# Optimization experiments

Hardware: AMD Instinct MI355X
Metric: run time of the kernel (lower is better)

## Reference

```python
import jax, jax.numpy as jnp
import numpy as np

B, S, D, H = 2, 2048, 1024, 16
DK = D // H


def setup_inputs() -> dict:
    key = jax.random.key(0)
    ks = jax.random.split(key, 11)
    std = 1.0 / np.sqrt(D)
    inp = {
        "query": jax.random.normal(ks[0], (B, S, D), jnp.float32),
        "key": jax.random.normal(ks[1], (B, S, D), jnp.float32),
        "value": jax.random.normal(ks[2], (B, S, D), jnp.float32),
        # True = masked position (torch masked_fill semantics); causal mask
        "mask": jnp.triu(jnp.ones((1, 1, S, S), jnp.bool_), k=1),
        "Wq": jax.random.normal(ks[3], (D, D), jnp.float32) * std,
        "bq": jnp.zeros((D,), jnp.float32),
        "Wk": jax.random.normal(ks[4], (D, D), jnp.float32) * std,
        "bk": jnp.zeros((D,), jnp.float32),
        "Wv": jax.random.normal(ks[5], (D, D), jnp.float32) * std,
        "bv": jnp.zeros((D,), jnp.float32),
        "Wo": jax.random.normal(ks[6], (D, D), jnp.float32) * std,
        "bo": jnp.zeros((D,), jnp.float32),
    }
    return inp


def _split_heads(x):
    b, s, _ = x.shape
    return x.reshape(b, s, H, DK).transpose(0, 2, 1, 3)  # [b, H, s, dk]


def reference(query, key, value, mask, Wq, bq, Wk, bk, Wv, bv, Wo, bo):
    q = _split_heads(query @ Wq + bq)
    k = _split_heads(key @ Wk + bk)
    v = _split_heads(value @ Wv + bv)
    scale = 1.0 / (DK ** 0.5)
    logits = jnp.einsum("bhqd,bhkd->bhqk", q, k) * scale
    logits = jnp.where(mask, -1.0e9, logits)
    w = jax.nn.softmax(logits, axis=-1)
    att = jnp.einsum("bhqk,bhkd->bhqd", w, v)  # [B, H, S, dk]
    # NOTE: faithful to the original bug -- view() without permuting heads back,
    # i.e. a raw row-major reshape [B,H,S,dk] -> [B,S,H*dk].
    att = att.reshape(att.shape[0], att.shape[2], -1)
    out = att @ Wo + bo
    return out
```

## Files before the change

### kernel.cpp

```cpp
#include <hip/hip_runtime.h>
#include <hip/hip_bf16.h>

typedef __hip_bfloat16 bf16;
typedef __attribute__((ext_vector_type(8))) short bf16x8;
typedef __attribute__((ext_vector_type(4))) float f32x4;

constexpr int Bc  = 2;
constexpr int Sc  = 2048;
constexpr int Dc  = 1024;
constexpr int Hc  = 16;
constexpr int DKc = 64;

__device__ __forceinline__ float bfbits2f(unsigned short u) {
  return __uint_as_float(((unsigned)u) << 16);
}
__device__ __forceinline__ unsigned short f2bfbits(float x) {
  bf16 h = __float2bfloat16(x);
  return *reinterpret_cast<unsigned short*>(&h);
}
__device__ __forceinline__ void store1_dyn(char* base, size_t ei, int isf32, float v) {
  if (isf32) *reinterpret_cast<float*>(base + ei * 4) = v;
  else       *reinterpret_cast<bf16*>(base + ei * 2) = __float2bfloat16(v);
}
__device__ __forceinline__ float fast_exp2(float x) {
  return __builtin_amdgcn_exp2f(x);
}
__device__ __forceinline__ uint4 pack8(const float4& a, const float4& b) {
  uint4 r;
  r.x = (unsigned)f2bfbits(a.x) | ((unsigned)f2bfbits(a.y) << 16);
  r.y = (unsigned)f2bfbits(a.z) | ((unsigned)f2bfbits(a.w) << 16);
  r.z = (unsigned)f2bfbits(b.x) | ((unsigned)f2bfbits(b.y) << 16);
  r.w = (unsigned)f2bfbits(b.z) | ((unsigned)f2bfbits(b.w) << 16);
  return r;
}
__device__ __forceinline__ void gld16(const void* g, void* l) {
  __builtin_amdgcn_global_load_lds(
      (const __attribute__((address_space(1))) unsigned int*)g,
      (__attribute__((address_space(3))) unsigned int*)l, 16, 0, 0);
}

__global__ void detect_dtype(const unsigned short* __restrict__ q, int* __restrict__ flag) {
  __shared__ int cnt[256];
  const int tid = threadIdx.x;
  int c = 0;
  for (int i = tid; i < 2048; i += 256) {
    const unsigned short u = q[i];
    const int e = (u >> 7) & 0xFF;
    if (e >= 134 || e <= 90) ++c;
  }
  cnt[tid] = c;
  __syncthreads();
  for (int s = 128; s > 0; s >>= 1) {
    if (tid < s) cnt[tid] += cnt[tid + s];
    __syncthreads();
  }
  if (tid == 0) flag[0] = (cnt[0] > 64) ? 1 : 0;
}

__global__ __launch_bounds__(256)
void prep_convert(const char* __restrict__ A0, const char* __restrict__ A1,
                  const char* __restrict__ A2, bf16* __restrict__ B0,
                  bf16* __restrict__ B1, bf16* __restrict__ B2,
                  const int* __restrict__ flagp) {
  const int dyn = flagp[0];
  const int z = blockIdx.y;
  const char* src = (z == 0) ? A0 : (z == 1) ? A1 : A2;
  bf16* dst = (z == 0) ? B0 : (z == 1) ? B1 : B2;
  const size_t n = (size_t)4096 * Dc;
  const size_t stride = (size_t)512 * 256 * 8;
  for (size_t i = ((size_t)blockIdx.x * 256 + threadIdx.x) * 8; i < n; i += stride) {
    uint4 u;
    if (dyn) {
      const float4* p = reinterpret_cast<const float4*>(src + i * 4);
      u = pack8(p[0], p[1]);
    } else {
      u = *reinterpret_cast<const uint4*>(src + i * 2);
    }
    *reinterpret_cast<uint4*>(dst + i) = u;
  }
}

__global__ __launch_bounds__(256)
void transpose_w4(const char* __restrict__ W0, const char* __restrict__ W1,
                  const char* __restrict__ W2, const char* __restrict__ W3,
                  unsigned short* __restrict__ Wt_all, const int* __restrict__ flagp) {
  __shared__ unsigned short T[64][72];
  const int dyn = flagp[0];
  const int z = blockIdx.z;
  const char* W = (z == 0) ? W0 : (z == 1) ? W1 : (z == 2) ? W2 : W3;
  unsigned short* Wt = Wt_all + (size_t)z * Dc * Dc;
  const int tid = threadIdx.x;
  const int n0 = blockIdx.x * 64, k0 = blockIdx.y * 64;
  const int r = tid >> 2, c16 = (tid & 3) * 16;

  unsigned short us[16];
  if (dyn) {
    const float4* p = reinterpret_cast<const float4*>(
        W + ((size_t)(k0 + r) * Dc + n0 + c16) * 4);
    const float4 f0 = p[0], f1 = p[1], f2 = p[2], f3 = p[3];
    const float fv[16] = {f0.x, f0.y, f0.z, f0.w, f1.x, f1.y, f1.z, f1.w,
                          f2.x, f2.y, f2.z, f2.w, f3.x, f3.y, f3.z, f3.w};
#pragma unroll
    for (int i = 0; i < 16; ++i) us[i] = f2bfbits(fv[i]);
  } else {
    const ushort4* p = reinterpret_cast<const ushort4*>(
        W + ((size_t)(k0 + r) * Dc + n0 + c16) * 2);
    const ushort4 u0 = p[0], u1 = p[1], u2 = p[2], u3 = p[3];
    us[0] = u0.x;  us[1] = u0.y;  us[2] = u0.z;  us[3] = u0.w;
    us[4] = u1.x;  us[5] = u1.y;  us[6] = u1.z;  us[7] = u1.w;
    us[8] = u2.x;  us[9] = u2.y;  us[10] = u2.z; us[11] = u2.w;
    us[12] = u3.x; us[13] = u3.y; us[14] = u3.z; us[15] = u3.w;
  }
#pragma unroll
  for (int i = 0; i < 16; ++i) T[r][c16 + i] = us[i];
  __syncthreads();

  unsigned vs[8];
#pragma unroll
  for (int i = 0; i < 8; ++i)
    vs[i] = (unsigned)T[c16 + 2 * i][r] | ((unsigned)T[c16 + 2 * i + 1][r] << 16);
  uint4* op = reinterpret_cast<uint4*>(Wt + (size_t)(n0 + r) * Dc + k0 + c16);
  op[0] = make_uint4(vs[0], vs[1], vs[2], vs[3]);
  op[1] = make_uint4(vs[4], vs[5], vs[6], vs[7]);
}

__global__ void conv_bias(const char* __restrict__ b0, const char* __restrict__ b1,
                          const char* __restrict__ b2, const char* __restrict__ b3,
                          unsigned short* __restrict__ out, const int* __restrict__ flagp) {
  const int dyn = flagp[0];
  const char* src = (blockIdx.x == 0) ? b0 : (blockIdx.x == 1) ? b1
                    : (blockIdx.x == 2) ? b2 : b3;
  for (int i = threadIdx.x; i < Dc; i += 256) {
    float v = dyn ? reinterpret_cast<const float*>(src)[i]
                  : bfbits2f(reinterpret_cast<const unsigned short*>(src)[i]);
    out[blockIdx.x * Dc + i] = f2bfbits(v);
  }
}

__global__ __launch_bounds__(256)
void qkv_gemm_async(const bf16* __restrict__ A0, const bf16* __restrict__ A1,
                    const bf16* __restrict__ A2,
                    const unsigned short* __restrict__ Wt_all,
                    const unsigned short* __restrict__ bias_all,
                    bf16* __restrict__ C0, bf16* __restrict__ C1,
                    bf16* __restrict__ C2) {
  constexpr int K = Dc, N = Dc;
  __shared__ __align__(16) unsigned short At[128 * 32];
  __shared__ __align__(16) unsigned short Bt[128 * 32];

  const int z = blockIdx.z;
  const bf16* A = (z == 0) ? A0 : (z == 1) ? A1 : A2;
  bf16* C = (z == 0) ? C0 : (z == 1) ? C1 : C2;
  const float scale = (z == 0) ? 0.18033688011112042f : 1.0f;
  const unsigned short* Wt = Wt_all + (size_t)z * Dc * Dc;
  const unsigned short* bias = bias_all + z * Dc;

  const int tid = threadIdx.x;
  const int m0 = blockIdx.x * 128, n0 = blockIdx.y * 128;
  const int w = tid >> 6, lane = tid & 63;
  const int lo16 = lane & 15, quad = lane >> 4;
  const int wm = (w >> 1) * 64, wn = (w & 1) * 64;

  unsigned short* ldsA = &At[w * 1024 + lane * 8];
  unsigned short* ldsB = &Bt[w * 1024 + lane * 8];
  const bf16* gA = A + (size_t)(m0 + w * 32 + (lane >> 2)) * K + (lane & 3) * 8;
  const unsigned short* gB = Wt + (size_t)(n0 + w * 32 + (lane >> 2)) * K + (lane & 3) * 8;

  f32x4 acc[4][4] = {};

  for (int k0 = 0; k0 < K; k0 += 32) {
    gld16(gA + k0, ldsA);
    gld16(gA + (size_t)16 * K + k0, ldsA + 512);
    gld16(gB + k0, ldsB);
    gld16(gB + (size_t)16 * K + k0, ldsB + 512);
    __syncthreads();

    bf16x8 afr[4], bfr[4];
#pragma unroll
    for (int mt = 0; mt < 4; ++mt)
      afr[mt] = *reinterpret_cast<const bf16x8*>(&At[(wm + mt * 16 + lo16) * 32 + quad * 8]);
#pragma unroll
    for (int nt = 0; nt < 4; ++nt)
      bfr[nt] = *reinterpret_cast<const bf16x8*>(&Bt[(wn + nt * 16 + lo16) * 32 + quad * 8]);
#pragma unroll
    for (int mt = 0; mt < 4; ++mt)
#pragma unroll
      for (int nt = 0; nt < 4; ++nt)
        acc[mt][nt] = __builtin_amdgcn_mfma_f32_16x16x32_bf16(afr[mt], bfr[nt],
                                                              acc[mt][nt], 0, 0, 0);
    __syncthreads();
  }

  float bv[4];
#pragma unroll
  for (int nt = 0; nt < 4; ++nt)
    bv[nt] = bfbits2f(bias[n0 + wn + nt * 16 + lo16]);
#pragma unroll
  for (int mt = 0; mt < 4; ++mt)
#pragma unroll
    for (int r = 0; r < 4; ++r) {
      const int row = m0 + wm + mt * 16 + quad * 4 + r;
#pragma unroll
      for (int nt = 0; nt < 4; ++nt) {
        const int col = n0 + wn + nt * 16 + lo16;
        C[(size_t)row * N + col] = __float2bfloat16((acc[mt][nt][r] + bv[nt]) * scale);
      }
    }
}

__global__ __launch_bounds__(256)
void qkv_gemm(const char* __restrict__ A0, const char* __restrict__ A1,
              const char* __restrict__ A2, const unsigned short* __restrict__ Wt_all,
              const unsigned short* __restrict__ bias_all,
              bf16* __restrict__ C0, bf16* __restrict__ C1, bf16* __restrict__ C2,
              const int* __restrict__ flagp) {
  constexpr int K = Dc, N = Dc;
  __shared__ __align__(16) unsigned short At[128][32];
  __shared__ __align__(16) unsigned short Bt[128][32];

  const int z = blockIdx.z;
  const char* A = (z == 0) ? A0 : (z == 1) ? A1 : A2;
  bf16* C = (z == 0) ? C0 : (z == 1) ? C1 : C2;
  const float scale = (z == 0) ? 0.18033688011112042f : 1.0f;
  const unsigned short* Wt = Wt_all + (size_t)z * Dc * Dc;
  const unsigned short* bias = bias_all + z * Dc;
  const int af = flagp[0];

  const int tid = threadIdx.x;
  const int m0 = blockIdx.x * 128, n0 = blockIdx.y * 128;
  const int w = tid >> 6, lane = tid & 63;
  const int lo16 = lane & 15, quad = lane >> 4;
  const int wm = (w >> 1) * 64, wn = (w & 1) * 64;
  const int sr = tid >> 1, sh = (tid & 1) * 16;

  f32x4 acc[4][4] = {};

  for (int k0 = 0; k0 < K; k0 += 32) {
    uint4 a_lo, a_hi;
    if (af) {
      const float4* p = reinterpret_cast<const float4*>(
          A + ((size_t)(m0 + sr) * K + k0 + sh) * 4);
      a_lo = pack8(p[0], p[1]);
      a_hi = pack8(p[2], p[3]);
    } else {
      const uint4* p = reinterpret_cast<const uint4*>(
          A + ((size_t)(m0 + sr) * K + k0 + sh) * 2);
      a_lo = p[0];
      a_hi = p[1];
    }
    const uint4* wp = reinterpret_cast<const uint4*>(Wt + (size_t)(n0 + sr) * K + k0 + sh);
    const uint4 b_lo = wp[0], b_hi = wp[1];

    __syncthreads();
    *reinterpret_cast<uint4*>(&At[sr][sh])     = a_lo;
    *reinterpret_cast<uint4*>(&At[sr][sh + 8]) = a_hi;
    *reinterpret_cast<uint4*>(&Bt[sr][sh])     = b_lo;
    *reinterpret_cast<uint4*>(&Bt[sr][sh + 8]) = b_hi;
    __syncthreads();

    bf16x8 afr[4], bfr[4];
#pragma unroll
    for (int mt = 0; mt < 4; ++mt)
      afr[mt] = *reinterpret_cast<const bf16x8*>(&At[wm + mt * 16 + lo16][quad * 8]);
#pragma unroll
    for (int nt = 0; nt < 4; ++nt)
      bfr[nt] = *reinterpret_cast<const bf16x8*>(&Bt[wn + nt * 16 + lo16][quad * 8]);
#pragma unroll
    for (int mt = 0; mt < 4; ++mt)
#pragma unroll
      for (int nt = 0; nt < 4; ++nt)
        acc[mt][nt] = __builtin_amdgcn_mfma_f32_16x16x32_bf16(afr[mt], bfr[nt],
                                                              acc[mt][nt], 0, 0, 0);
  }

  float bv[4];
#pragma unroll
  for (int nt = 0; nt < 4; ++nt)
    bv[nt] = bfbits2f(bias[n0 + wn + nt * 16 + lo16]);
#pragma unroll
  for (int mt = 0; mt < 4; ++mt)
#pragma unroll
    for (int r = 0; r < 4; ++r) {
      const int row = m0 + wm + mt * 16 + quad * 4 + r;
#pragma unroll
      for (int nt = 0; nt < 4; ++nt) {
        const int col = n0 + wn + nt * 16 + lo16;
        C[(size_t)row * N + col] = __float2bfloat16((acc[mt][nt][r] + bv[nt]) * scale);
      }
    }
}

__global__ __launch_bounds__(256)
void out_gemm_async(const bf16* __restrict__ A, const unsigned short* __restrict__ Wt,
                    const unsigned short* __restrict__ bias, char* __restrict__ C,
                    const int* __restrict__ flagp) {
  constexpr int K = Dc, N = Dc;
  __shared__ __align__(16) unsigned short At[64 * 32];
  __shared__ __align__(16) unsigned short Bt[128 * 32];

  const int cf = flagp[0];
  const int tid = threadIdx.x;
  const int m0 = blockIdx.x * 64, n0 = blockIdx.y * 128;
  const int w = tid >> 6, lane = tid & 63;
  const int lo16 = lane & 15, quad = lane >> 4;
  const int wm = (w >> 1) * 32, wn = (w & 1) * 64;

  unsigned short* ldsA = &At[w * 512 + lane * 8];
  unsigned short* ldsB = &Bt[w * 1024 + lane * 8];
  const bf16* gA = A + (size_t)(m0 + w * 16 + (lane >> 2)) * K + (lane & 3) * 8;
  const unsigned short* gB = Wt + (size_t)(n0 + w * 32 + (lane >> 2)) * K + (lane & 3) * 8;

  f32x4 acc[2][4] = {};

  for (int k0 = 0; k0 < K; k0 += 32) {
    gld16(gA + k0, ldsA);
    gld16(gB + k0, ldsB);
    gld16(gB + (size_t)16 * K + k0, ldsB + 512);
    __syncthreads();

    bf16x8 afr[2], bfr[4];
#pragma unroll
    for (int mt = 0; mt < 2; ++mt)
      afr[mt] = *reinterpret_cast<const bf16x8*>(&At[(wm + mt * 16 + lo16) * 32 + quad * 8]);
#pragma unroll
    for (int nt = 0; nt < 4; ++nt)
      bfr[nt] = *reinterpret_cast<const bf16x8*>(&Bt[(wn + nt * 16 + lo16) * 32 + quad * 8]);
#pragma unroll
    for (int mt = 0; mt < 2; ++mt)
#pragma unroll
      for (int nt = 0; nt < 4; ++nt)
        acc[mt][nt] = __builtin_amdgcn_mfma_f32_16x16x32_bf16(afr[mt], bfr[nt],
                                                              acc[mt][nt], 0, 0, 0);
    __syncthreads();
  }

  float bv[4];
#pragma unroll
  for (int nt = 0; nt < 4; ++nt)
    bv[nt] = bfbits2f(bias[n0 + wn + nt * 16 + lo16]);
#pragma unroll
  for (int mt = 0; mt < 2; ++mt)
#pragma unroll
    for (int r = 0; r < 4; ++r) {
      const int row = m0 + wm + mt * 16 + quad * 4 + r;
#pragma unroll
      for (int nt = 0; nt < 4; ++nt) {
        const int col = n0 + wn + nt * 16 + lo16;
        store1_dyn(C, (size_t)row * N + col, cf, acc[mt][nt][r] + bv[nt]);
      }
    }
}

__global__ __launch_bounds__(256)
void attn_mfma(const bf16* __restrict__ Q, const bf16* __restrict__ K,
               const bf16* __restrict__ V, bf16* __restrict__ O) {
  __shared__ __align__(16) unsigned short Kt[64][72];
  __shared__ __align__(16) unsigned short Vt[64][72];
  __shared__ __align__(16) unsigned short St[4][16][72];
  __shared__ float Li[4][16];

  const int hb = blockIdx.x & 31;
  const int bx = blockIdx.x >> 5;
  const int b = hb >> 4, h = hb & 15;
  const int tid = threadIdx.x;
  const int w = tid >> 6;
  const int lane = tid & 63;
  const int lo16 = lane & 15, quad = lane >> 4;
  const size_t hd = (size_t)h * DKc;

  const int kr = tid >> 2, kc = (tid & 3) * 16;
  const int vk = (tid & 31) * 2, vd0 = (tid >> 5) * 8;

  for (int pi = 0; pi < 2; ++pi) {
    const int qt = pi ? (31 - bx) : bx;
    const int q0 = qt * 64;

    const bf16* qrow = Q + ((size_t)(b * Sc + q0 + w * 16 + lo16)) * Dc + hd;
    const bf16x8 qa0 = *reinterpret_cast<const bf16x8*>(qrow + quad * 8);
    const bf16x8 qa1 = *reinterpret_cast<const bf16x8*>(qrow + 32 + quad * 8);

    f32x4 oacc[4] = {f32x4{0,0,0,0}, f32x4{0,0,0,0}, f32x4{0,0,0,0}, f32x4{0,0,0,0}};
    float lsum = 0.f;
    const int qg = q0 + w * 16 + lo16;

    for (int t = 0; t <= qt; ++t) {
      const int kt = t * 64;
      __syncthreads();
      {
        const bf16* kp = K + ((size_t)(b * Sc + kt + kr)) * Dc + hd + kc;
        const uint4 k0v = *reinterpret_cast<const uint4*>(kp);
        const uint4 k1v = *reinterpret_cast<const uint4*>(kp + 8);
        *reinterpret_cast<uint4*>(&Kt[kr][kc])     = k0v;
        *reinterpret_cast<uint4*>(&Kt[kr][kc + 8]) = k1v;
      }
      {
        const bf16* vbase = V + ((size_t)(b * Sc + kt + vk)) * Dc + hd + vd0;
        const uint4 ra = *reinterpret_cast<const uint4*>(vbase);
        const uint4 rb = *reinterpret_cast<const uint4*>(vbase + Dc);
        *reinterpret_cast<unsigned*>(&Vt[vd0 + 0][vk]) = (ra.x & 0xffffu) | (rb.x << 16);
        *reinterpret_cast<unsigned*>(&Vt[vd0 + 1][vk]) = (ra.x >> 16)     | (rb.x & 0xffff0000u);
        *reinterpret_cast<unsigned*>(&Vt[vd0 + 2][vk]) = (ra.y & 0xffffu) | (rb.y << 16);
        *reinterpret_cast<unsigned*>(&Vt[vd0 + 3][vk]) = (ra.y >> 16)     | (rb.y & 0xffff0000u);
        *reinterpret_cast<unsigned*>(&Vt[vd0 + 4][vk]) = (ra.z & 0xffffu) | (rb.z << 16);
        *reinterpret_cast<unsigned*>(&Vt[vd0 + 5][vk]) = (ra.z >> 16)     | (rb.z & 0xffff0000u);
        *reinterpret_cast<unsigned*>(&Vt[vd0 + 6][vk]) = (ra.w & 0xffffu) | (rb.w << 16);
        *reinterpret_cast<unsigned*>(&Vt[vd0 + 7][vk]) = (ra.w >> 16)     | (rb.w & 0xffff0000u);
      }
      __syncthreads();

      f32x4 s[4] = {f32x4{0,0,0,0}, f32x4{0,0,0,0}, f32x4{0,0,0,0}, f32x4{0,0,0,0}};
#pragma unroll
      for (int ct = 0; ct < 4; ++ct) {
        const bf16x8 ka0 = *reinterpret_cast<const bf16x8*>(&Kt[ct * 16 + lo16][quad * 8]);
        const bf16x8 ka1 = *reinterpret_cast<const bf16x8*>(&Kt[ct * 16 + lo16][32 + quad * 8]);
        s[ct] = __builtin_amdgcn_mfma_f32_16x16x32_bf16(ka0, qa0, s[ct], 0, 0, 0);
        s[ct] = __builtin_amdgcn_mfma_f32_16x16x32_bf16(ka1, qa1, s[ct], 0, 0, 0);
      }

      if (kt + 63 > q0 + w * 16) {
#pragma unroll
        for (int ct = 0; ct < 4; ++ct)
#pragma unroll
          for (int r = 0; r < 4; ++r)
            if (kt + ct * 16 + quad * 4 + r > qg) s[ct][r] = -1e9f;
      }

#pragma unroll
      for (int ct = 0; ct < 4; ++ct) {
        const float p0 = fast_exp2(fminf(s[ct][0], 43.f));
        const float p1 = fast_exp2(fminf(s[ct][1], 43.f));
        const float p2 = fast_exp2(fminf(s[ct][2], 43.f));
        const float p3 = fast_exp2(fminf(s[ct][3], 43.f));
        lsum += (p0 + p1) + (p2 + p3);
        uint2 pk;
        pk.x = (unsigned)f2bfbits(p0) | ((unsigned)f2bfbits(p1) << 16);
        pk.y = (unsigned)f2bfbits(p2) | ((unsigned)f2bfbits(p3) << 16);
        *reinterpret_cast<uint2*>(&St[w][lo16][ct * 16 + quad * 4]) = pk;
      }

      const bf16x8 pa0 = *reinterpret_cast<const bf16x8*>(&St[w][lo16][quad * 8]);
      const bf16x8 pa1 = *reinterpret_cast<const bf16x8*>(&St[w][lo16][32 + quad * 8]);
#pragma unroll
      for (int ct = 0; ct < 4; ++ct) {
        const bf16x8 vb0 = *reinterpret_cast<const bf16x8*>(&Vt[ct * 16 + lo16][quad * 8]);
        const bf16x8 vb1 = *reinterpret_cast<const bf16x8*>(&Vt[ct * 16 + lo16][32 + quad * 8]);
        oacc[ct] = __builtin_amdgcn_mfma_f32_16x16x32_bf16(pa0, vb0, oacc[ct], 0, 0, 0);
        oacc[ct] = __builtin_amdgcn_mfma_f32_16x16x32_bf16(pa1, vb1, oacc[ct], 0, 0, 0);
      }
    }

    lsum += __shfl_xor(lsum, 16);
    lsum += __shfl_xor(lsum, 32);
    if (quad == 0) Li[w][lo16] = 1.f / lsum;
    __builtin_amdgcn_wave_barrier();
    const f32x4 invv = *reinterpret_cast<const f32x4*>(&Li[w][quad * 4]);

#pragma unroll
    for (int r = 0; r < 4; ++r) {
      bf16* op = O + (((size_t)(b * Hc + h) * Sc) + q0 + w * 16 + quad * 4 + r) * DKc + lo16;
#pragma unroll
      for (int ct = 0; ct < 4; ++ct)
        op[ct * 16] = __float2bfloat16(oacc[ct][r] * invv[r]);
    }
  }
}

extern "C" void kernel_launch(void* const* d_in, const int* in_sizes, int n_in,
                              void* d_out, int out_size, void* d_ws, size_t ws_size,
                              hipStream_t stream) {
  (void)in_sizes; (void)out_size;
  const char* query = (const char*)d_in[0];
  const char* key_  = (const char*)d_in[1];
  const char* value = (const char*)d_in[2];
  const int wb = n_in - 8;
  const char* Wq = (const char*)d_in[wb + 0];
  const char* bq = (const char*)d_in[wb + 1];
  const char* Wk = (const char*)d_in[wb + 2];
  const char* bk = (const char*)d_in[wb + 3];
  const char* Wv = (const char*)d_in[wb + 4];
  const char* bv = (const char*)d_in[wb + 5];
  const char* Wo = (const char*)d_in[wb + 6];
  const char* bo = (const char*)d_in[wb + 7];

  char* ws = (char*)d_ws;
  bf16* Qs  = (bf16*)(ws);
  bf16* Ks  = (bf16*)(ws + ((size_t)8  << 20));
  bf16* Vs  = (bf16*)(ws + ((size_t)16 << 20));
  bf16* att = (bf16*)(ws + ((size_t)24 << 20));
  unsigned short* Wt_all = (unsigned short*)(ws + ((size_t)32 << 20));
  unsigned short* bb_all = (unsigned short*)(ws + ((size_t)40 << 20));
  int* flag = (int*)(ws + ((size_t)40 << 20) + 16384);
  bf16* Qb = (bf16*)(ws + ((size_t)42 << 20));
  bf16* Kb = (bf16*)(ws + ((size_t)50 << 20));
  bf16* Vb = (bf16*)(ws + ((size_t)58 << 20));
  const bool big_ws = ws_size >= ((size_t)66 << 20);

  detect_dtype<<<1, 256, 0, stream>>>((const unsigned short*)query, flag);

  transpose_w4<<<dim3(16, 16, 4), 256, 0, stream>>>(Wq, Wk, Wv, Wo, Wt_all, flag);
  conv_bias<<<4, 256, 0, stream>>>(bq, bk, bv, bo, bb_all, flag);

  if (big_ws) {
    prep_convert<<<dim3(512, 3), 256, 0, stream>>>(query, key_, value, Qb, Kb, Vb, flag);
    qkv_gemm_async<<<dim3(32, 8, 3), 256, 0, stream>>>(Qb, Kb, Vb, Wt_all, bb_all,
                                                       Qs, Ks, Vs);
  } else {
    qkv_gemm<<<dim3(32, 8, 3), 256, 0, stream>>>(query, key_, value, Wt_all, bb_all,
                                                 Qs, Ks, Vs, flag);
  }

  attn_mfma<<<dim3(512), 256, 0, stream>>>(Qs, Ks, Vs, att);

  out_gemm_async<<<dim3(64, 8), 256, 0, stream>>>(att, Wt_all + (size_t)3 * Dc * Dc,
                                                  bb_all + 3 * Dc, (char*)d_out, flag);
}
```

Measured before the change: 241.7 us.

## Merge prep kernels, split attention into one q-tile per block, pack bf16 pairs

Fuses the weight transpose, bias conversion and input conversion into a single prep_all launch to cut launch overhead. The attention kernel now handles one query tile per block (1024 blocks instead of 512 blocks each doing a paired light/heavy tile), ordered in a zigzag so the causal work stays balanced across waves. It also drops the fminf clamp before exp2 and uses packed float2-to-bf16 conversion. These changes add parallelism but lose the explicit pairing balance, and removing the clamp relies on the logits never overflowing.

After: 237.7 us. No clear change (-1.6%).

```diff
diff --git a/kernel.cpp b/kernel.cpp
--- a/kernel.cpp
+++ b/kernel.cpp
@@ -25,12 +25,16 @@
 __device__ __forceinline__ float fast_exp2(float x) {
   return __builtin_amdgcn_exp2f(x);
 }
+__device__ __forceinline__ unsigned pkbf16(float a, float b) {
+  __hip_bfloat162 h = __float22bfloat162_rn(make_float2(a, b));
+  return *reinterpret_cast<unsigned*>(&h);
+}
 __device__ __forceinline__ uint4 pack8(const float4& a, const float4& b) {
   uint4 r;
-  r.x = (unsigned)f2bfbits(a.x) | ((unsigned)f2bfbits(a.y) << 16);
-  r.y = (unsigned)f2bfbits(a.z) | ((unsigned)f2bfbits(a.w) << 16);
-  r.z = (unsigned)f2bfbits(b.x) | ((unsigned)f2bfbits(b.y) << 16);
-  r.w = (unsigned)f2bfbits(b.z) | ((unsigned)f2bfbits(b.w) << 16);
+  r.x = pkbf16(a.x, a.y);
+  r.y = pkbf16(a.z, a.w);
+  r.z = pkbf16(b.x, b.y);
+  r.w = pkbf16(b.z, b.w);
   return r;
 }
 __device__ __forceinline__ void gld16(const void* g, void* l) {
@@ -58,82 +62,82 @@
 }
 
 __global__ __launch_bounds__(256)
-void prep_convert(const char* __restrict__ A0, const char* __restrict__ A1,
-                  const char* __restrict__ A2, bf16* __restrict__ B0,
-                  bf16* __restrict__ B1, bf16* __restrict__ B2,
-                  const int* __restrict__ flagp) {
-  const int dyn = flagp[0];
-  const int z = blockIdx.y;
-  const char* src = (z == 0) ? A0 : (z == 1) ? A1 : A2;
-  bf16* dst = (z == 0) ? B0 : (z == 1) ? B1 : B2;
-  const size_t n = (size_t)4096 * Dc;
-  const size_t stride = (size_t)512 * 256 * 8;
-  for (size_t i = ((size_t)blockIdx.x * 256 + threadIdx.x) * 8; i < n; i += stride) {
-    uint4 u;
-    if (dyn) {
-      const float4* p = reinterpret_cast<const float4*>(src + i * 4);
-      u = pack8(p[0], p[1]);
-    } else {
-      u = *reinterpret_cast<const uint4*>(src + i * 2);
-    }
-    *reinterpret_cast<uint4*>(dst + i) = u;
-  }
-}
-
-__global__ __launch_bounds__(256)
-void transpose_w4(const char* __restrict__ W0, const char* __restrict__ W1,
-                  const char* __restrict__ W2, const char* __restrict__ W3,
-                  unsigned short* __restrict__ Wt_all, const int* __restrict__ flagp) {
+void prep_all(const char* __restrict__ W0, const char* __restrict__ W1,
+              const char* __restrict__ W2, const char* __restrict__ W3,
+              unsigned short* __restrict__ Wt_all,
+              const char* __restrict__ b0, const char* __restrict__ b1,
+              const char* __restrict__ b2, const char* __restrict__ b3,
+              unsigned short* __restrict__ bb_all,
+              const char* __restrict__ A0, const char* __restrict__ A1,
+              const char* __restrict__ A2, bf16* __restrict__ B0,
+              bf16* __restrict__ B1, bf16* __restrict__ B2,
+              const int* __restrict__ flagp) {
   __shared__ unsigned short T[64][72];
   const int dyn = flagp[0];
-  const int z = blockIdx.z;
-  const char* W = (z == 0) ? W0 : (z == 1) ? W1 : (z == 2) ? W2 : W3;
-  unsigned short* Wt = Wt_all + (size_t)z * Dc * Dc;
+  const int id = blockIdx.x;
   const int tid = threadIdx.x;
-  const int n0 = blockIdx.x * 64, k0 = blockIdx.y * 64;
-  const int r = tid >> 2, c16 = (tid & 3) * 16;
-
-  unsigned short us[16];
-  if (dyn) {
-    const float4* p = reinterpret_cast<const float4*>(
-        W + ((size_t)(k0 + r) * Dc + n0 + c16) * 4);
-    const float4 f0 = p[0], f1 = p[1], f2 = p[2], f3 = p[3];
-    const float fv[16] = {f0.x, f0.y, f0.z, f0.w, f1.x, f1.y, f1.z, f1.w,
-                          f2.x, f2.y, f2.z, f2.w, f3.x, f3.y, f3.z, f3.w};
-#pragma unroll
-    for (int i = 0; i < 16; ++i) us[i] = f2bfbits(fv[i]);
+
+  if (id < 1024) {
+    const int z = id >> 8, rem = id & 255;
+    const int n0 = (rem & 15) * 64, k0 = (rem >> 4) * 64;
+    const char* W = (z == 0) ? W0 : (z == 1) ? W1 : (z == 2) ? W2 : W3;
+    unsigned short* Wt = Wt_all + (size_t)z * Dc * Dc;
+    const int r = tid >> 2, c16 = (tid & 3) * 16;
+
+    unsigned short us[16];
+    if (dyn) {
+      const float4* p = reinterpret_cast<const float4*>(
+          W + ((size_t)(k0 + r) * Dc + n0 + c16) * 4);
+      const float4 f0 = p[0], f1 = p[1], f2 = p[2], f3 = p[3];
+      const float fv[16] = {f0.x, f0.y, f0.z, f0.w, f1.x, f1.y, f1.z, f1.w,
+                            f2.x, f2.y, f2.z, f2.w, f3.x, f3.y, f3.z, f3.w};
+#pragma unroll
+      for (int i = 0; i < 16; ++i) us[i] = f2bfbits(fv[i]);
+    } else {
+      const ushort4* p = reinterpret_cast<const ushort4*>(
+          W + ((size_t)(k0 + r) * Dc + n0 + c16) * 2);
+      const ushort4 u0 = p[0], u1 = p[1], u2 = p[2], u3 = p[3];
+      us[0] = u0.x;  us[1] = u0.y;  us[2] = u0.z;  us[3] = u0.w;
+      us[4] = u1.x;  us[5] = u1.y;  us[6] = u1.z;  us[7] = u1.w;
+      us[8] = u2.x;  us[9] = u2.y;  us[10] = u2.z; us[11] = u2.w;
+      us[12] = u3.x; us[13] = u3.y; us[14] = u3.z; us[15] = u3.w;
+    }
+#pragma unroll
+    for (int i = 0; i < 16; ++i) T[r][c16 + i] = us[i];
+    __syncthreads();
+
+    unsigned vs[8];
+#pragma unroll
+    for (int i = 0; i < 8; ++i)
+      vs[i] = (unsigned)T[c16 + 2 * i][r] | ((unsigned)T[c16 + 2 * i + 1][r] << 16);
+    uint4* op = reinterpret_cast<uint4*>(Wt + (size_t)(n0 + r) * Dc + k0 + c16);
+    op[0] = make_uint4(vs[0], vs[1], vs[2], vs[3]);
+    op[1] = make_uint4(vs[4], vs[5], vs[6], vs[7]);
+  } else if (id < 2560) {
+    const int j = id - 1024;
+    const int z = j >> 9, x = j & 511;
+    const char* src = (z == 0) ? A0 : (z == 1) ? A1 : A2;
+    bf16* dst = (z == 0) ? B0 : (z == 1) ? B1 : B2;
+    const size_t n = (size_t)4096 * Dc;
+    const size_t stride = (size_t)512 * 256 * 8;
+    for (size_t i = ((size_t)x * 256 + tid) * 8; i < n; i += stride) {
+      uint4 u;
+      if (dyn) {
+        const float4* p = reinterpret_cast<const float4*>(src + i * 4);
+        u = pack8(p[0], p[1]);
+      } else {
+        u = *reinterpret_cast<const uint4*>(src + i * 2);
+      }
+      *reinterpret_cast<uint4*>(dst + i) = u;
+    }
   } else {
-    const ushort4* p = reinterpret_cast<const ushort4*>(
-        W + ((size_t)(k0 + r) * Dc + n0 + c16) * 2);
-    const ushort4 u0 = p[0], u1 = p[1], u2 = p[2], u3 = p[3];
-    us[0] = u0.x;  us[1] = u0.y;  us[2] = u0.z;  us[3] = u0.w;
-    us[4] = u1.x;  us[5] = u1.y;  us[6] = u1.z;  us[7] = u1.w;
-    us[8] = u2.x;  us[9] = u2.y;  us[10] = u2.z; us[11] = u2.w;
-    us[12] = u3.x; us[13] = u3.y; us[14] = u3.z; us[15] = u3.w;
-  }
-#pragma unroll
-  for (int i = 0; i < 16; ++i) T[r][c16 + i] = us[i];
-  __syncthreads();
-
-  unsigned vs[8];
-#pragma unroll
-  for (int i = 0; i < 8; ++i)
-    vs[i] = (unsigned)T[c16 + 2 * i][r] | ((unsigned)T[c16 + 2 * i + 1][r] << 16);
-  uint4* op = reinterpret_cast<uint4*>(Wt + (size_t)(n0 + r) * Dc + k0 + c16);
-  op[0] = make_uint4(vs[0], vs[1], vs[2], vs[3]);
-  op[1] = make_uint4(vs[4], vs[5], vs[6], vs[7]);
-}
-
-__global__ void conv_bias(const char* __restrict__ b0, const char* __restrict__ b1,
-                          const char* __restrict__ b2, const char* __restrict__ b3,
-                          unsigned short* __restrict__ out, const int* __restrict__ flagp) {
-  const int dyn = flagp[0];
-  const char* src = (blockIdx.x == 0) ? b0 : (blockIdx.x == 1) ? b1
-                    : (blockIdx.x == 2) ? b2 : b3;
-  for (int i = threadIdx.x; i < Dc; i += 256) {
-    float v = dyn ? reinterpret_cast<const float*>(src)[i]
-                  : bfbits2f(reinterpret_cast<const unsigned short*>(src)[i]);
-    out[blockIdx.x * Dc + i] = f2bfbits(v);
+    const int x = id - 2560;
+    const char* src = (x == 0) ? b0 : (x == 1) ? b1 : (x == 2) ? b2 : b3;
+    for (int i = tid; i < Dc; i += 256) {
+      float v = dyn ? reinterpret_cast<const float*>(src)[i]
+                    : bfbits2f(reinterpret_cast<const unsigned short*>(src)[i]);
+      bb_all[x * Dc + i] = f2bfbits(v);
+    }
   }
 }
 
@@ -360,8 +364,11 @@
   __shared__ float Li[4][16];
 
   const int hb = blockIdx.x & 31;
-  const int bx = blockIdx.x >> 5;
+  const int i  = blockIdx.x >> 5;
+  const int g = i >> 3, r0 = i & 7;
+  const int qt = (g == 0) ? r0 : (g == 1) ? 15 - r0 : (g == 2) ? 16 + r0 : 31 - r0;
   const int b = hb >> 4, h = hb & 15;
+  const int q0 = qt * 64;
   const int tid = threadIdx.x;
   const int w = tid >> 6;
   const int lane = tid & 63;
@@ -371,97 +378,92 @@
   const int kr = tid >> 2, kc = (tid & 3) * 16;
   const int vk = (tid & 31) * 2, vd0 = (tid >> 5) * 8;
 
-  for (int pi = 0; pi < 2; ++pi) {
-    const int qt = pi ? (31 - bx) : bx;
-    const int q0 = qt * 64;
-
-    const bf16* qrow = Q + ((size_t)(b * Sc + q0 + w * 16 + lo16)) * Dc + hd;
-    const bf16x8 qa0 = *reinterpret_cast<const bf16x8*>(qrow + quad * 8);
-    const bf16x8 qa1 = *reinterpret_cast<const bf16x8*>(qrow + 32 + quad * 8);
-
-    f32x4 oacc[4] = {f32x4{0,0,0,0}, f32x4{0,0,0,0}, f32x4{0,0,0,0}, f32x4{0,0,0,0}};
-    float lsum = 0.f;
-    const int qg = q0 + w * 16 + lo16;
-
-    for (int t = 0; t <= qt; ++t) {
-      const int kt = t * 64;
-      __syncthreads();
-      {
-        const bf16* kp = K + ((size_t)(b * Sc + kt + kr)) * Dc + hd + kc;
-        const uint4 k0v = *reinterpret_cast<const uint4*>(kp);
-        const uint4 k1v = *reinterpret_cast<const uint4*>(kp + 8);
-        *reinterpret_cast<uint4*>(&Kt[kr][kc])     = k0v;
-        *reinterpret_cast<uint4*>(&Kt[kr][kc + 8]) = k1v;
-      }
-      {
-        const bf16* vbase = V + ((size_t)(b * Sc + kt + vk)) * Dc + hd + vd0;
-        const uint4 ra = *reinterpret_cast<const uint4*>(vbase);
-        const uint4 rb = *reinterpret_cast<const uint4*>(vbase + Dc);
-        *reinterpret_cast<unsigned*>(&Vt[vd0 + 0][vk]) = (ra.x & 0xffffu) | (rb.x << 16);
-        *reinterpret_cast<unsigned*>(&Vt[vd0 + 1][vk]) = (ra.x >> 16)     | (rb.x & 0xffff0000u);
-        *reinterpret_cast<unsigned*>(&Vt[vd0 + 2][vk]) = (ra.y & 0xffffu) | (rb.y << 16);
-        *reinterpret_cast<unsigned*>(&Vt[vd0 + 3][vk]) = (ra.y >> 16)     | (rb.y & 0xffff0000u);
-        *reinterpret_cast<unsigned*>(&Vt[vd0 + 4][vk]) = (ra.z & 0xffffu) | (rb.z << 16);
-        *reinterpret_cast<unsigned*>(&Vt[vd0 + 5][vk]) = (ra.z >> 16)     | (rb.z & 0xffff0000u);
-        *reinterpret_cast<unsigned*>(&Vt[vd0 + 6][vk]) = (ra.w & 0xffffu) | (rb.w << 16);
-        *reinterpret_cast<unsigned*>(&Vt[vd0 + 7][vk]) = (ra.w >> 16)     | (rb.w & 0xffff0000u);
-      }
-      __syncthreads();
-
-      f32x4 s[4] = {f32x4{0,0,0,0}, f32x4{0,0,0,0}, f32x4{0,0,0,0}, f32x4{0,0,0,0}};
-#pragma unroll
-      for (int ct = 0; ct < 4; ++ct) {
-        const bf16x8 ka0 = *reinterpret_cast<const bf16x8*>(&Kt[ct * 16 + lo16][quad * 8]);
-        const bf16x8 ka1 = *reinterpret_cast<const bf16x8*>(&Kt[ct * 16 + lo16][32 + quad * 8]);
-        s[ct] = __builtin_amdgcn_mfma_f32_16x16x32_bf16(ka0, qa0, s[ct], 0, 0, 0);
-        s[ct] = __builtin_amdgcn_mfma_f32_16x16x32_bf16(ka1, qa1, s[ct], 0, 0, 0);
-      }
-
-      if (kt + 63 > q0 + w * 16) {
-#pragma unroll
-        for (int ct = 0; ct < 4; ++ct)
-#pragma unroll
-          for (int r = 0; r < 4; ++r)
-            if (kt + ct * 16 + quad * 4 + r > qg) s[ct][r] = -1e9f;
-      }
-
-#pragma unroll
-      for (int ct = 0; ct < 4; ++ct) {
-        const float p0 = fast_exp2(fminf(s[ct][0], 43.f));
-        const float p1 = fast_exp2(fminf(s[ct][1], 43.f));
-        const float p2 = fast_exp2(fminf(s[ct][2], 43.f));
-        const float p3 = fast_exp2(fminf(s[ct][3], 43.f));
-        lsum += (p0 + p1) + (p2 + p3);
-        uint2 pk;
-        pk.x = (unsigned)f2bfbits(p0) | ((unsigned)f2bfbits(p1) << 16);
-        pk.y = (unsigned)f2bfbits(p2) | ((unsigned)f2bfbits(p3) << 16);
-        *reinterpret_cast<uint2*>(&St[w][lo16][ct * 16 + quad * 4]) = pk;
-      }
-
-      const bf16x8 pa0 = *reinterpret_cast<const bf16x8*>(&St[w][lo16][quad * 8]);
-      const bf16x8 pa1 = *reinterpret_cast<const bf16x8*>(&St[w][lo16][32 + quad * 8]);
-#pragma unroll
-      for (int ct = 0; ct < 4; ++ct) {
-        const bf16x8 vb0 = *reinterpret_cast<const bf16x8*>(&Vt[ct * 16 + lo16][quad * 8]);
-        const bf16x8 vb1 = *reinterpret_cast<const bf16x8*>(&Vt[ct * 16 + lo16][32 + quad * 8]);
-        oacc[ct] = __builtin_amdgcn_mfma_f32_16x16x32_bf16(pa0, vb0, oacc[ct], 0, 0, 0);
-        oacc[ct] = __builtin_amdgcn_mfma_f32_16x16x32_bf16(pa1, vb1, oacc[ct], 0, 0, 0);
-      }
-    }
-
-    lsum += __shfl_xor(lsum, 16);
-    lsum += __shfl_xor(lsum, 32);
-    if (quad == 0) Li[w][lo16] = 1.f / lsum;
-    __builtin_amdgcn_wave_barrier();
-    const f32x4 invv = *reinterpret_cast<const f32x4*>(&Li[w][quad * 4]);
-
-#pragma unroll
-    for (int r = 0; r < 4; ++r) {
-      bf16* op = O + (((size_t)(b * Hc + h) * Sc) + q0 + w * 16 + quad * 4 + r) * DKc + lo16;
+  const bf16* qrow = Q + ((size_t)(b * Sc + q0 + w * 16 + lo16)) * Dc + hd;
+  const bf16x8 qa0 = *reinterpret_cast<const bf16x8*>(qrow + quad * 8);
+  const bf16x8 qa1 = *reinterpret_cast<const bf16x8*>(qrow + 32 + quad * 8);
+
+  f32x4 oacc[4] = {f32x4{0,0,0,0}, f32x4{0,0,0,0}, f32x4{0,0,0,0}, f32x4{0,0,0,0}};
+  float lsum = 0.f;
+  const int qg = q0 + w * 16 + lo16;
+
+  for (int t = 0; t <= qt; ++t) {
+    const int kt = t * 64;
+    __syncthreads();
+    {
+      const bf16* kp = K + ((size_t)(b * Sc + kt + kr)) * Dc + hd + kc;
+      const uint4 k0v = *reinterpret_cast<const uint4*>(kp);
+      const uint4 k1v = *reinterpret_cast<const uint4*>(kp + 8);
+      *reinterpret_cast<uint4*>(&Kt[kr][kc])     = k0v;
+      *reinterpret_cast<uint4*>(&Kt[kr][kc + 8]) = k1v;
+    }
+    {
+      const bf16* vbase = V + ((size_t)(b * Sc + kt + vk)) * Dc + hd + vd0;
+      const uint4 ra = *reinterpret_cast<const uint4*>(vbase);
+      const uint4 rb = *reinterpret_cast<const uint4*>(vbase + Dc);
+      *reinterpret_cast<unsigned*>(&Vt[vd0 + 0][vk]) = (ra.x & 0xffffu) | (rb.x << 16);
+      *reinterpret_cast<unsigned*>(&Vt[vd0 + 1][vk]) = (ra.x >> 16)     | (rb.x & 0xffff0000u);
+      *reinterpret_cast<unsigned*>(&Vt[vd0 + 2][vk]) = (ra.y & 0xffffu) | (rb.y << 16);
+      *reinterpret_cast<unsigned*>(&Vt[vd0 + 3][vk]) = (ra.y >> 16)     | (rb.y & 0xffff0000u);
+      *reinterpret_cast<unsigned*>(&Vt[vd0 + 4][vk]) = (ra.z & 0xffffu) | (rb.z << 16);
+      *reinterpret_cast<unsigned*>(&Vt[vd0 + 5][vk]) = (ra.z >> 16)     | (rb.z & 0xffff0000u);
+      *reinterpret_cast<unsigned*>(&Vt[vd0 + 6][vk]) = (ra.w & 0xffffu) | (rb.w << 16);
+      *reinterpret_cast<unsigned*>(&Vt[vd0 + 7][vk]) = (ra.w >> 16)     | (rb.w & 0xffff0000u);
+    }
+    __syncthreads();
+
+    f32x4 s[4] = {f32x4{0,0,0,0}, f32x4{0,0,0,0}, f32x4{0,0,0,0}, f32x4{0,0,0,0}};
+#pragma unroll
+    for (int ct = 0; ct < 4; ++ct) {
+      const bf16x8 ka0 = *reinterpret_cast<const bf16x8*>(&Kt[ct * 16 + lo16][quad * 8]);
+      const bf16x8 ka1 = *reinterpret_cast<const bf16x8*>(&Kt[ct * 16 + lo16][32 + quad * 8]);
+      s[ct] = __builtin_amdgcn_mfma_f32_16x16x32_bf16(ka0, qa0, s[ct], 0, 0, 0);
+      s[ct] = __builtin_amdgcn_mfma_f32_16x16x32_bf16(ka1, qa1, s[ct], 0, 0, 0);
+    }
+
+    if (kt + 63 > q0 + w * 16) {
 #pragma unroll
       for (int ct = 0; ct < 4; ++ct)
-        op[ct * 16] = __float2bfloat16(oacc[ct][r] * invv[r]);
-    }
+#pragma unroll
+        for (int r = 0; r < 4; ++r)
+          if (kt + ct * 16 + quad * 4 + r > qg) s[ct][r] = -1e9f;
+    }
+
+#pragma unroll
+    for (int ct = 0; ct < 4; ++ct) {
+      const float p0 = fast_exp2(s[ct][0]);
+      const float p1 = fast_exp2(s[ct][1]);
+      const float p2 = fast_exp2(s[ct][2]);
+      const float p3 = fast_exp2(s[ct][3]);
+      lsum += (p0 + p1) + (p2 + p3);
+      uint2 pk;
+      pk.x = pkbf16(p0, p1);
+      pk.y = pkbf16(p2, p3);
+      *reinterpret_cast<uint2*>(&St[w][lo16][ct * 16 + quad * 4]) = pk;
+    }
+
+    const bf16x8 pa0 = *reinterpret_cast<const bf16x8*>(&St[w][lo16][quad * 8]);
+    const bf16x8 pa1 = *reinterpret_cast<const bf16x8*>(&St[w][lo16][32 + quad * 8]);
+#pragma unroll
+    for (int ct = 0; ct < 4; ++ct) {
+      const bf16x8 vb0 = *reinterpret_cast<const bf16x8*>(&Vt[ct * 16 + lo16][quad * 8]);
+      const bf16x8 vb1 = *reinterpret_cast<const bf16x8*>(&Vt[ct * 16 + lo16][32 + quad * 8]);
+      oacc[ct] = __builtin_amdgcn_mfma_f32_16x16x32_bf16(pa0, vb0, oacc[ct], 0, 0, 0);
+      oacc[ct] = __builtin_amdgcn_mfma_f32_16x16x32_bf16(pa1, vb1, oacc[ct], 0, 0, 0);
+    }
+  }
+
+  lsum += __shfl_xor(lsum, 16);
+  lsum += __shfl_xor(lsum, 32);
+  if (quad == 0) Li[w][lo16] = 1.f / lsum;
+  __builtin_amdgcn_wave_barrier();
+  const f32x4 invv = *reinterpret_cast<const f32x4*>(&Li[w][quad * 4]);
+
+#pragma unroll
+  for (int r = 0; r < 4; ++r) {
+    bf16* op = O + (((size_t)(b * Hc + h) * Sc) + q0 + w * 16 + quad * 4 + r) * DKc + lo16;
+#pragma unroll
+    for (int ct = 0; ct < 4; ++ct)
+      op[ct * 16] = __float2bfloat16(oacc[ct][r] * invv[r]);
   }
 }
 
@@ -497,19 +499,20 @@
 
   detect_dtype<<<1, 256, 0, stream>>>((const unsigned short*)query, flag);
 
-  transpose_w4<<<dim3(16, 16, 4), 256, 0, stream>>>(Wq, Wk, Wv, Wo, Wt_all, flag);
-  conv_bias<<<4, 256, 0, stream>>>(bq, bk, bv, bo, bb_all, flag);
-
   if (big_ws) {
-    prep_convert<<<dim3(512, 3), 256, 0, stream>>>(query, key_, value, Qb, Kb, Vb, flag);
+    prep_all<<<2564, 256, 0, stream>>>(Wq, Wk, Wv, Wo, Wt_all, bq, bk, bv, bo,
+                                       bb_all, query, key_, value, Qb, Kb, Vb, flag);
     qkv_gemm_async<<<dim3(32, 8, 3), 256, 0, stream>>>(Qb, Kb, Vb, Wt_all, bb_all,
                                                        Qs, Ks, Vs);
   } else {
+    prep_all<<<1028, 256, 0, stream>>>(Wq, Wk, Wv, Wo, Wt_all, bq, bk, bv, bo,
+                                       bb_all, query, key_, value,
+                                       (bf16*)att, (bf16*)att, (bf16*)att, flag);
     qkv_gemm<<<dim3(32, 8, 3), 256, 0, stream>>>(query, key_, value, Wt_all, bb_all,
                                                  Qs, Ks, Vs, flag);
   }
 
-  attn_mfma<<<dim3(512), 256, 0, stream>>>(Qs, Ks, Vs, att);
+  attn_mfma<<<dim3(1024), 256, 0, stream>>>(Qs, Ks, Vs, att);
 
   out_gemm_async<<<dim3(64, 8), 256, 0, stream>>>(att, Wt_all + (size_t)3 * Dc * Dc,
                                                   bb_all + 3 * Dc, (char*)d_out, flag);
```
